# Optimization experiments

Hardware: AMD Instinct MI355X
Metric: run time of the kernel (lower is better)

## Reference

```python
import jax, jax.numpy as jnp
import numpy as np

B, C, N = 4, 256, 2048
H = 8
HD = C // H  # head_dim = 32


def setup_inputs() -> dict:
    key = jax.random.key(0)
    ks = jax.random.split(key, 5)
    s = 1.0 / np.sqrt(C)
    return {
        "x": jax.random.normal(ks[0], (B, C, 3, N), dtype=jnp.float32),
        "Wq": jax.random.normal(ks[1], (C, C), dtype=jnp.float32) * s,
        "Wk": jax.random.normal(ks[2], (C, C), dtype=jnp.float32) * s,
        "Wv": jax.random.normal(ks[3], (C, C), dtype=jnp.float32) * s,
        "Wo": jax.random.normal(ks[4], (C, C), dtype=jnp.float32) * s,
    }


def _vn_linear(W, x):
    # nn.Linear over channel axis: out[b,o,d,n] = sum_c W[o,c] x[b,c,d,n]
    return jnp.einsum('oc,bcdn->bodn', W, x)


def _heads(t):
    # [B,C,3,N] -> [B,H,N,HD,3]
    return t.reshape(B, H, HD, 3, N).transpose(0, 1, 4, 2, 3)


def reference(x, Wq, Wk, Wv, Wo):
    q = _heads(_vn_linear(Wq, x))
    k = _heads(_vn_linear(Wk, x))
    v = _heads(_vn_linear(Wv, x))
    # energy contracts over (head_dim, 3)
    energy = jnp.einsum('bhnci,bhmci->bhnm', q, k)
    attn = jax.nn.softmax(energy / np.sqrt(HD), axis=-1)
    out = jnp.einsum('bhnm,bhmci->bhnci', attn, v)
    # [B,H,N,HD,3] -> [B,C,3,N]
    out = out.transpose(0, 1, 3, 4, 2).reshape(B, C, 3, N)
    out = _vn_linear(Wo, out)
    return out + x
```

## Files before the change

kernel.cpp:

```cpp
#include <hip/hip_runtime.h>
#include <hip/hip_bf16.h>
#include <cmath>


typedef unsigned short u16;
typedef unsigned int   u32;
typedef u16   u16x8  __attribute__((ext_vector_type(8)));
typedef short s16x8  __attribute__((ext_vector_type(8)));
typedef float f32x4  __attribute__((ext_vector_type(4)));
typedef float f32x16 __attribute__((ext_vector_type(16)));

namespace {
constexpr int Nc = 2048, Fc = 96;
constexpr float SCALE_LOG2 = 0.17677669529663687f * 1.4426950408889634f;
constexpr int KP = 104;
constexpr int VP = 40;
constexpr int VOFF = 32 * KP;
constexpr int SBUF = VOFF + 96 * VP;
}

__device__ inline float fast_exp2(float x) {
#if __has_builtin(__builtin_amdgcn_exp2f)
    return __builtin_amdgcn_exp2f(x);
#else
    return exp2f(x);
#endif
}

__device__ inline u16 f2bf(float x) {
    union { float f; unsigned u; } v; v.f = x;
    unsigned r = v.u + 0x7FFFu + ((v.u >> 16) & 1u);
    return (u16)(r >> 16);
}

__global__ __launch_bounds__(256) void wconv_kernel(
    const float* __restrict__ Wq, const float* __restrict__ Wk,
    const float* __restrict__ Wv, const float* __restrict__ Wo,
    u16* __restrict__ Wb)
{
    const int id = blockIdx.x * 256 + threadIdx.x;
    const int base = id * 8;
    const int o = base >> 8, c = base & 255;
    const int sel = o >> 8, ol = o & 255;
    const float* src = (sel == 0) ? Wq : (sel == 1) ? Wk : (sel == 2) ? Wv : Wo;
    const float sc = (sel == 0) ? SCALE_LOG2 : 1.0f;
    const float4 a = *(const float4*)&src[(size_t)ol * 256 + c];
    const float4 b = *(const float4*)&src[(size_t)ol * 256 + c + 4];
    u16x8 r;
    r[0]=f2bf(a.x*sc); r[1]=f2bf(a.y*sc); r[2]=f2bf(a.z*sc); r[3]=f2bf(a.w*sc);
    r[4]=f2bf(b.x*sc); r[5]=f2bf(b.y*sc); r[6]=f2bf(b.z*sc); r[7]=f2bf(b.w*sc);
    *(u16x8*)&Wb[(size_t)o * 256 + c] = r;
}

__global__ __launch_bounds__(256) void xt_kernel(
    const float* __restrict__ x, u16* __restrict__ xt)
{
    const int nt = blockIdx.x, ct = blockIdx.y, bi = blockIdx.z;
    const int b = bi / 3, i = bi % 3;
    const int t = (int)threadIdx.x;
    const int n0 = nt * 64, c0 = ct * 64;

    __shared__ u16 tile[64][72];

    const int n_l = t & 63;
#pragma unroll
    for (int it = 0; it < 16; ++it) {
        const int c_l = (t >> 6) + it * 4;
        tile[n_l][c_l] =
            f2bf(x[(((size_t)(b * 256 + c0 + c_l)) * 3 + i) * Nc + n0 + n_l]);
    }
    __syncthreads();
#pragma unroll
    for (int it = 0; it < 2; ++it) {
        const int idx = t + it * 256;
        const int nn = idx >> 3, part = idx & 7;
        *(u16x8*)&xt[((size_t)bi * Nc + n0 + nn) * 256 + c0 + part * 8] =
            *(const u16x8*)&tile[nn][part * 8];
    }
}

__global__ __launch_bounds__(256) void qkv_gemm_kernel(
    const u16* __restrict__ xt, const u16* __restrict__ wb,
    u16* __restrict__ Qt, u16* __restrict__ Kt, u16* __restrict__ Vf)
{
    const int nt = blockIdx.x;
    const int wy = blockIdx.y;
    const int bi = blockIdx.z;
    const int b = bi / 3, i = bi % 3;
    const int wsel = wy >> 1, ot = wy & 1;

    const u16* xs = xt + ((size_t)bi * Nc + nt * 128) * 256;
    const u16* ws = wb + (size_t)(wsel * 256 + ot * 128) * 256;

    __shared__ u16 xl[128][40];
    __shared__ u16 wl[128][40];

    const int t = (int)threadIdx.x;
    const int wv = t >> 6, lane = t & 63;
    const int g = lane >> 4, c16 = lane & 15;
    const int wr = wv >> 1, wc = wv & 1;

    f32x4 acc[4][4];
#pragma unroll
    for (int mi = 0; mi < 4; ++mi)
#pragma unroll
        for (int ni = 0; ni < 4; ++ni)
#pragma unroll
            for (int r = 0; r < 4; ++r) acc[mi][ni][r] = 0.f;

    for (int ks = 0; ks < 8; ++ks) {
        __syncthreads();
#pragma unroll
        for (int it = 0; it < 2; ++it) {
            const int idx = t + it * 256;
            const int row = idx >> 2, part = idx & 3;
            *(u16x8*)&xl[row][part * 8] =
                *(const u16x8*)&xs[(size_t)row * 256 + ks * 32 + part * 8];
            *(u16x8*)&wl[row][part * 8] =
                *(const u16x8*)&ws[(size_t)row * 256 + ks * 32 + part * 8];
        }
        __syncthreads();

        s16x8 af[4], bf[4];
        if (wsel < 2) {
#pragma unroll
            for (int mi = 0; mi < 4; ++mi) af[mi] = *(const s16x8*)&xl[wr*64 + mi*16 + c16][g*8];
#pragma unroll
            for (int ni = 0; ni < 4; ++ni) bf[ni] = *(const s16x8*)&wl[wc*64 + ni*16 + c16][g*8];
        } else {
#pragma unroll
            for (int mi = 0; mi < 4; ++mi) af[mi] = *(const s16x8*)&wl[wr*64 + mi*16 + c16][g*8];
#pragma unroll
            for (int ni = 0; ni < 4; ++ni) bf[ni] = *(const s16x8*)&xl[wc*64 + ni*16 + c16][g*8];
        }
#pragma unroll
        for (int mi = 0; mi < 4; ++mi)
#pragma unroll
            for (int ni = 0; ni < 4; ++ni)
                acc[mi][ni] = __builtin_amdgcn_mfma_f32_16x16x32_bf16(
                    af[mi], bf[ni], acc[mi][ni], 0, 0, 0);
    }

    if (wsel < 2) {
        u16* dst = wsel ? Kt : Qt;
#pragma unroll
        for (int mi = 0; mi < 4; ++mi)
#pragma unroll
            for (int ni = 0; ni < 4; ++ni) {
                const int o = ot * 128 + wc * 64 + ni * 16 + c16;
                const int h = o >> 5, cw = o & 31;
#pragma unroll
                for (int r = 0; r < 4; ++r) {
                    const int n = nt * 128 + wr * 64 + mi * 16 + g * 4 + r;
                    dst[((size_t)(b * 8 + h) * Nc + n) * Fc + i * 32 + cw] =
                        f2bf(acc[mi][ni][r]);
                }
            }
    } else {
#pragma unroll
        for (int mi = 0; mi < 4; ++mi)
#pragma unroll
            for (int ni = 0; ni < 4; ++ni) {
                const int n = nt * 128 + wc * 64 + ni * 16 + c16;
#pragma unroll
                for (int r = 0; r < 4; ++r) {
                    const int o = ot * 128 + wr * 64 + mi * 16 + g * 4 + r;
                    const int h = o >> 5, cw = o & 31;
                    Vf[((size_t)(b * 8 + h) * Fc + i * 32 + cw) * Nc + n] =
                        f2bf(acc[mi][ni][r]);
                }
            }
    }
}

__global__ __launch_bounds__(256) void attn_mfma_kernel(
    const u16* __restrict__ Qt, const u16* __restrict__ Kt,
    const u16* __restrict__ Vf, u16* __restrict__ aot)
{
    const int bid = (int)blockIdx.x;
    const int lid = (bid & 7) * 64 + (bid >> 3);
    const int bh = lid >> 4;
    const int qt = lid & 15;

    const int t_   = (int)threadIdx.x;
    const int wq   = t_ >> 6;
    const int lane = t_ & 63;
    const int ql   = lane & 31;
    const int hi   = lane >> 5;

    __shared__ u16 sbuf[3 * SBUF];

    const int qb = qt * 128 + wq * 32;

    s16x8 bq[6];
#pragma unroll
    for (int s6 = 0; s6 < 6; ++s6)
        bq[s6] = *(const s16x8*)&Qt[((size_t)bh * Nc + qb + ql) * Fc + s6 * 16 + hi * 8];

    const u16* g_cur[3]; int g_str[3], g_dst[3];
#pragma unroll
    for (int it = 0; it < 3; ++it) {
        const int c = t_ + it * 256;
        if (c < 384) {
            const int row = c / 12, part = c - row * 12;
            g_cur[it] = Kt + ((size_t)bh * Nc + row) * Fc + part * 8;
            g_str[it] = 32 * Fc;
            g_dst[it] = row * KP + part * 8;
        } else {
            const int c2 = c - 384, f = c2 >> 2, part = c2 & 3;
            g_cur[it] = Vf + ((size_t)bh * Fc + f) * Nc + part * 8;
            g_str[it] = 32;
            g_dst[it] = VOFF + f * VP + part * 8;
        }
    }

    f32x16 acc[3];
#pragma unroll
    for (int ft = 0; ft < 3; ++ft)
#pragma unroll
        for (int r = 0; r < 16; ++r) acc[ft][r] = 0.f;
    float lacc[8];
#pragma unroll
    for (int r = 0; r < 8; ++r) lacc[r] = 0.f;

    u16* b0 = sbuf;
    u16* b1 = sbuf + SBUF;
    u16* b2 = sbuf + 2 * SBUF;

    u16x8 sreg[3];
#pragma unroll
    for (int it = 0; it < 3; ++it) { sreg[it] = *(const u16x8*)g_cur[it]; g_cur[it] += g_str[it]; }
#pragma unroll
    for (int it = 0; it < 3; ++it) *(u16x8*)&b0[g_dst[it]] = sreg[it];
#pragma unroll
    for (int it = 0; it < 3; ++it) { sreg[it] = *(const u16x8*)g_cur[it]; g_cur[it] += g_str[it]; }
    __syncthreads();

    f32x16 svE, svO;
#pragma unroll
    for (int r = 0; r < 16; ++r) svE[r] = 0.f;
#pragma unroll
    for (int s6 = 0; s6 < 6; ++s6) {
        const s16x8 ka = *(const s16x8*)&b0[ql * KP + s6 * 16 + hi * 8];
        svE = __builtin_amdgcn_mfma_f32_32x32x16_bf16(ka, bq[s6], svE, 0, 0, 0);
    }
#pragma unroll
    for (int it = 0; it < 3; ++it) *(u16x8*)&b1[g_dst[it]] = sreg[it];
#pragma unroll
    for (int it = 0; it < 3; ++it) { sreg[it] = *(const u16x8*)g_cur[it]; g_cur[it] += g_str[it]; }
    __syncthreads();

    u16 *bA = b0, *bB = b1, *bC = b2;

    auto body = [&](int t, f32x16& SC, f32x16& SN) {
        if (t < 63) {
#pragma unroll
            for (int r = 0; r < 16; ++r) SN[r] = 0.f;
#pragma unroll
            for (int s6 = 0; s6 < 6; ++s6) {
                const s16x8 ka = *(const s16x8*)&bB[ql * KP + s6 * 16 + hi * 8];
                SN = __builtin_amdgcn_mfma_f32_32x32x16_bf16(ka, bq[s6], SN, 0, 0, 0);
            }
        }
        if (t < 62) {
#pragma unroll
            for (int it = 0; it < 3; ++it) *(u16x8*)&bC[g_dst[it]] = sreg[it];
        }
        if (t < 61) {
#pragma unroll
            for (int it = 0; it < 3; ++it) { sreg[it] = *(const u16x8*)g_cur[it]; g_cur[it] += g_str[it]; }
        }

#pragma unroll
        for (int r = 0; r < 16; ++r) SC[r] = fast_exp2(SC[r]);
#pragma unroll
        for (int r = 0; r < 8; ++r) lacc[r] += SC[r] + SC[r + 8];

        u32 pk8[8];
#pragma unroll
        for (int j = 0; j < 8; ++j)
            asm("v_cvt_pk_bf16_f32 %0, %1, %2" : "=v"(pk8[j]) : "v"(SC[2*j]), "v"(SC[2*j+1]));
        asm volatile("v_permlane32_swap_b32 %0, %1" : "+v"(pk8[0]), "+v"(pk8[2]));
        asm volatile("v_permlane32_swap_b32 %0, %1" : "+v"(pk8[1]), "+v"(pk8[3]));
        asm volatile("v_permlane32_swap_b32 %0, %1" : "+v"(pk8[4]), "+v"(pk8[6]));
        asm volatile("v_permlane32_swap_b32 %0, %1" : "+v"(pk8[5]), "+v"(pk8[7]));
        union U { u32 w[4]; s16x8 v; } pb0, pb1;
        pb0.w[0]=pk8[0]; pb0.w[1]=pk8[1]; pb0.w[2]=pk8[2]; pb0.w[3]=pk8[3];
        pb1.w[0]=pk8[4]; pb1.w[1]=pk8[5]; pb1.w[2]=pk8[6]; pb1.w[3]=pk8[7];

#pragma unroll
        for (int ft = 0; ft < 3; ++ft) {
            const s16x8 va0 = *(const s16x8*)&bA[VOFF + (ft * 32 + ql) * VP + hi * 8];
            acc[ft] = __builtin_amdgcn_mfma_f32_32x32x16_bf16(va0, pb0.v, acc[ft], 0, 0, 0);
            const s16x8 va1 = *(const s16x8*)&bA[VOFF + (ft * 32 + ql) * VP + 16 + hi * 8];
            acc[ft] = __builtin_amdgcn_mfma_f32_32x32x16_bf16(va1, pb1.v, acc[ft], 0, 0, 0);
        }

        if (t < 63) __syncthreads();
    };

    for (int tb = 0; tb < 32; ++tb) {
        body(2 * tb, svE, svO);
        { u16* tmp = bA; bA = bB; bB = bC; bC = tmp; }
        body(2 * tb + 1, svO, svE);
        { u16* tmp = bA; bA = bB; bB = bC; bC = tmp; }
    }

    float l4[4];
#pragma unroll
    for (int r = 0; r < 4; ++r) l4[r] = lacc[r] + lacc[r + 4];
    const float l2a = l4[0] + l4[2], l2b = l4[1] + l4[3];
    float l_s = l2a + l2b;
    l_s += __shfl_xor(l_s, 32);
    const float inv = 1.f / l_s;

    __syncthreads();
    u16* ot = sbuf + wq * 3328;
#pragma unroll
    for (int ft = 0; ft < 3; ++ft)
#pragma unroll
        for (int r = 0; r < 16; ++r) {
            const int frow = (r & 3) + 8 * (r >> 2) + 4 * hi;
            ot[ql * 104 + ft * 32 + frow] = f2bf(acc[ft][r] * inv);
        }
    __syncthreads();

    u16x8 v6[6];
#pragma unroll
    for (int j = 0; j < 6; ++j)
        v6[j] = *(const u16x8*)&ot[ql * 104 + hi * 48 + j * 8];

    const int n = qb + ql;
    const int b_ = bh >> 3, h_ = bh & 7;
    const size_t base0 = ((size_t)(b_ * 3 + 0) * Nc + n) * 256 + h_ * 32;
    const size_t base1 = ((size_t)(b_ * 3 + 1) * Nc + n) * 256 + h_ * 32;
    const size_t base2 = ((size_t)(b_ * 3 + 2) * Nc + n) * 256 + h_ * 32;
    if (hi == 0) {
        *(u16x8*)&aot[base0 +  0] = v6[0];
        *(u16x8*)&aot[base0 +  8] = v6[1];
        *(u16x8*)&aot[base0 + 16] = v6[2];
        *(u16x8*)&aot[base0 + 24] = v6[3];
        *(u16x8*)&aot[base1 +  0] = v6[4];
        *(u16x8*)&aot[base1 +  8] = v6[5];
    } else {
        *(u16x8*)&aot[base1 + 16] = v6[0];
        *(u16x8*)&aot[base1 + 24] = v6[1];
        *(u16x8*)&aot[base2 +  0] = v6[2];
        *(u16x8*)&aot[base2 +  8] = v6[3];
        *(u16x8*)&aot[base2 + 16] = v6[4];
        *(u16x8*)&aot[base2 + 24] = v6[5];
    }
}

__global__ __launch_bounds__(256) void out_gemm_kernel(
    const u16* __restrict__ aot, const u16* __restrict__ wb,
    const float* __restrict__ x, float* __restrict__ out)
{
    const int nt = blockIdx.x, ot = blockIdx.y, bi = blockIdx.z;
    const int b = bi / 3, i = bi % 3;

    const u16* bs = aot + ((size_t)bi * Nc + nt * 128) * 256;
    const u16* ws = wb + (size_t)(768 + ot * 128) * 256;

    __shared__ u16 al[128][40];
    __shared__ u16 wl[128][40];

    const int t = (int)threadIdx.x;
    const int wv = t >> 6, lane = t & 63;
    const int g = lane >> 4, c16 = lane & 15;
    const int wr = wv >> 1, wc = wv & 1;

    f32x4 acc[4][4];
#pragma unroll
    for (int mi = 0; mi < 4; ++mi)
#pragma unroll
        for (int ni = 0; ni < 4; ++ni)
#pragma unroll
            for (int r = 0; r < 4; ++r) acc[mi][ni][r] = 0.f;

    for (int ks = 0; ks < 8; ++ks) {
        __syncthreads();
#pragma unroll
        for (int it = 0; it < 2; ++it) {
            const int idx = t + it * 256;
            const int row = idx >> 2, part = idx & 3;
            *(u16x8*)&al[row][part * 8] =
                *(const u16x8*)&bs[(size_t)row * 256 + ks * 32 + part * 8];
            *(u16x8*)&wl[row][part * 8] =
                *(const u16x8*)&ws[(size_t)row * 256 + ks * 32 + part * 8];
        }
        __syncthreads();

        s16x8 af[4], bf[4];
#pragma unroll
        for (int mi = 0; mi < 4; ++mi) af[mi] = *(const s16x8*)&wl[wr*64 + mi*16 + c16][g*8];
#pragma unroll
        for (int ni = 0; ni < 4; ++ni) bf[ni] = *(const s16x8*)&al[wc*64 + ni*16 + c16][g*8];
#pragma unroll
        for (int mi = 0; mi < 4; ++mi)
#pragma unroll
            for (int ni = 0; ni < 4; ++ni)
                acc[mi][ni] = __builtin_amdgcn_mfma_f32_16x16x32_bf16(
                    af[mi], bf[ni], acc[mi][ni], 0, 0, 0);
    }

#pragma unroll
    for (int mi = 0; mi < 4; ++mi)
#pragma unroll
        for (int ni = 0; ni < 4; ++ni) {
            const int n = nt * 128 + wc * 64 + ni * 16 + c16;
#pragma unroll
            for (int r = 0; r < 4; ++r) {
                const int o = ot * 128 + wr * 64 + mi * 16 + g * 4 + r;
                const size_t idx = ((size_t)(b * 256 + o) * 3 + i) * Nc + n;
                out[idx] = x[idx] + acc[mi][ni][r];
            }
        }
}

extern "C" void kernel_launch(void* const* d_in, const int* in_sizes, int n_in,
                              void* d_out, int out_size, void* d_ws, size_t ws_size,
                              hipStream_t stream) {
    const float* x  = (const float*)d_in[0];
    const float* Wq = (const float*)d_in[1];
    const float* Wk = (const float*)d_in[2];
    const float* Wv = (const float*)d_in[3];
    const float* Wo = (const float*)d_in[4];
    float* out = (float*)d_out;

    const size_t E = (size_t)32 * Fc * Nc;
    u16* xt  = (u16*)d_ws;
    u16* wbw = xt + E;
    u16* qt  = wbw + 262144;
    u16* kt  = qt + E;
    u16* vf  = kt + E;
    u16* aot = vf + E;

    dim3 blk(256);
    wconv_kernel    <<<dim3(128),        blk, 0, stream>>>(Wq, Wk, Wv, Wo, wbw);
    xt_kernel       <<<dim3(32, 4, 12),  blk, 0, stream>>>(x, xt);
    qkv_gemm_kernel <<<dim3(16, 6, 12),  blk, 0, stream>>>(xt, wbw, qt, kt, vf);
    attn_mfma_kernel<<<dim3(512),        blk, 0, stream>>>(qt, kt, vf, aot);
    out_gemm_kernel <<<dim3(16, 2, 12),  blk, 0, stream>>>(aot, wbw, x, out);
}
```

Before: 124.9 us.

## Split attention over two key halves and merge partials in a combine kernel

The attention kernel now splits the key range into two halves, launching twice as many blocks that each process 1024 keys, and writes unnormalized-then-normalized partial outputs plus row sums to workspace. A new combine kernel weights the two partials by their softmax sums and writes the head-interleaved layout consumed by the output GEMM. The K/V pipeline is simplified from triple to double buffering with a launch bound hint for higher occupancy. This raises parallelism on 256 CUs but adds an extra kernel launch, extra global traffic for partials, and bf16 rounding of partials.

```diff
diff --git a/kernel.cpp b/kernel.cpp
--- a/kernel.cpp
+++ b/kernel.cpp
@@ -31,6 +31,10 @@
     union { float f; unsigned u; } v; v.f = x;
     unsigned r = v.u + 0x7FFFu + ((v.u >> 16) & 1u);
     return (u16)(r >> 16);
+}
+
+__device__ inline float bf2f(u16 x) {
+    union { unsigned u; float f; } v; v.u = ((unsigned)x) << 16; return v.f;
 }
 
 __global__ __launch_bounds__(256) void wconv_kernel(
@@ -173,14 +177,16 @@
     }
 }
 
-__global__ __launch_bounds__(256) void attn_mfma_kernel(
+__global__ __launch_bounds__(256, 4) void attn_mfma_kernel(
     const u16* __restrict__ Qt, const u16* __restrict__ Kt,
-    const u16* __restrict__ Vf, u16* __restrict__ aot)
+    const u16* __restrict__ Vf, u16* __restrict__ Ob, float* __restrict__ lP)
 {
     const int bid = (int)blockIdx.x;
-    const int lid = (bid & 7) * 64 + (bid >> 3);
-    const int bh = lid >> 4;
-    const int qt = lid & 15;
+    const int lid = (bid & 7) * 128 + (bid >> 3);
+    const int bh   = lid >> 5;
+    const int r5   = lid & 31;
+    const int qt   = r5 >> 1;
+    const int half = r5 & 1;
 
     const int t_   = (int)threadIdx.x;
     const int wq   = t_ >> 6;
@@ -188,9 +194,10 @@
     const int ql   = lane & 31;
     const int hi   = lane >> 5;
 
-    __shared__ u16 sbuf[3 * SBUF];
+    __shared__ u16 sbuf[2 * SBUF];
 
     const int qb = qt * 128 + wq * 32;
+    const int k0 = half * 1024;
 
     s16x8 bq[6];
 #pragma unroll
@@ -203,12 +210,12 @@
         const int c = t_ + it * 256;
         if (c < 384) {
             const int row = c / 12, part = c - row * 12;
-            g_cur[it] = Kt + ((size_t)bh * Nc + row) * Fc + part * 8;
+            g_cur[it] = Kt + ((size_t)bh * Nc + k0 + row) * Fc + part * 8;
             g_str[it] = 32 * Fc;
             g_dst[it] = row * KP + part * 8;
         } else {
             const int c2 = c - 384, f = c2 >> 2, part = c2 & 3;
-            g_cur[it] = Vf + ((size_t)bh * Fc + f) * Nc + part * 8;
+            g_cur[it] = Vf + ((size_t)bh * Fc + f) * Nc + k0 + part * 8;
             g_str[it] = 32;
             g_dst[it] = VOFF + f * VP + part * 8;
         }
@@ -223,63 +230,46 @@
 #pragma unroll
     for (int r = 0; r < 8; ++r) lacc[r] = 0.f;
 
-    u16* b0 = sbuf;
-    u16* b1 = sbuf + SBUF;
-    u16* b2 = sbuf + 2 * SBUF;
+    u16* bA = sbuf;
+    u16* bB = sbuf + SBUF;
 
     u16x8 sreg[3];
 #pragma unroll
     for (int it = 0; it < 3; ++it) { sreg[it] = *(const u16x8*)g_cur[it]; g_cur[it] += g_str[it]; }
 #pragma unroll
-    for (int it = 0; it < 3; ++it) *(u16x8*)&b0[g_dst[it]] = sreg[it];
+    for (int it = 0; it < 3; ++it) *(u16x8*)&bA[g_dst[it]] = sreg[it];
 #pragma unroll
     for (int it = 0; it < 3; ++it) { sreg[it] = *(const u16x8*)g_cur[it]; g_cur[it] += g_str[it]; }
     __syncthreads();
 
-    f32x16 svE, svO;
-#pragma unroll
-    for (int r = 0; r < 16; ++r) svE[r] = 0.f;
-#pragma unroll
-    for (int s6 = 0; s6 < 6; ++s6) {
-        const s16x8 ka = *(const s16x8*)&b0[ql * KP + s6 * 16 + hi * 8];
-        svE = __builtin_amdgcn_mfma_f32_32x32x16_bf16(ka, bq[s6], svE, 0, 0, 0);
-    }
-#pragma unroll
-    for (int it = 0; it < 3; ++it) *(u16x8*)&b1[g_dst[it]] = sreg[it];
-#pragma unroll
-    for (int it = 0; it < 3; ++it) { sreg[it] = *(const u16x8*)g_cur[it]; g_cur[it] += g_str[it]; }
-    __syncthreads();
-
-    u16 *bA = b0, *bB = b1, *bC = b2;
-
-    auto body = [&](int t, f32x16& SC, f32x16& SN) {
-        if (t < 63) {
-#pragma unroll
-            for (int r = 0; r < 16; ++r) SN[r] = 0.f;
-#pragma unroll
-            for (int s6 = 0; s6 < 6; ++s6) {
-                const s16x8 ka = *(const s16x8*)&bB[ql * KP + s6 * 16 + hi * 8];
-                SN = __builtin_amdgcn_mfma_f32_32x32x16_bf16(ka, bq[s6], SN, 0, 0, 0);
-            }
-        }
-        if (t < 62) {
-#pragma unroll
-            for (int it = 0; it < 3; ++it) *(u16x8*)&bC[g_dst[it]] = sreg[it];
-        }
-        if (t < 61) {
+    for (int kt = 0; kt < 32; ++kt) {
+        if (kt < 31) {
+#pragma unroll
+            for (int it = 0; it < 3; ++it) *(u16x8*)&bB[g_dst[it]] = sreg[it];
+        }
+        if (kt < 30) {
 #pragma unroll
             for (int it = 0; it < 3; ++it) { sreg[it] = *(const u16x8*)g_cur[it]; g_cur[it] += g_str[it]; }
         }
 
-#pragma unroll
-        for (int r = 0; r < 16; ++r) SC[r] = fast_exp2(SC[r]);
-#pragma unroll
-        for (int r = 0; r < 8; ++r) lacc[r] += SC[r] + SC[r + 8];
+        f32x16 sv;
+#pragma unroll
+        for (int r = 0; r < 16; ++r) sv[r] = 0.f;
+#pragma unroll
+        for (int s6 = 0; s6 < 6; ++s6) {
+            const s16x8 ka = *(const s16x8*)&bA[ql * KP + s6 * 16 + hi * 8];
+            sv = __builtin_amdgcn_mfma_f32_32x32x16_bf16(ka, bq[s6], sv, 0, 0, 0);
+        }
+
+#pragma unroll
+        for (int r = 0; r < 16; ++r) sv[r] = fast_exp2(sv[r]);
+#pragma unroll
+        for (int r = 0; r < 8; ++r) lacc[r] += sv[r] + sv[r + 8];
 
         u32 pk8[8];
 #pragma unroll
         for (int j = 0; j < 8; ++j)
-            asm("v_cvt_pk_bf16_f32 %0, %1, %2" : "=v"(pk8[j]) : "v"(SC[2*j]), "v"(SC[2*j+1]));
+            asm("v_cvt_pk_bf16_f32 %0, %1, %2" : "=v"(pk8[j]) : "v"(sv[2*j]), "v"(sv[2*j+1]));
         asm volatile("v_permlane32_swap_b32 %0, %1" : "+v"(pk8[0]), "+v"(pk8[2]));
         asm volatile("v_permlane32_swap_b32 %0, %1" : "+v"(pk8[1]), "+v"(pk8[3]));
         asm volatile("v_permlane32_swap_b32 %0, %1" : "+v"(pk8[4]), "+v"(pk8[6]));
@@ -296,59 +286,68 @@
             acc[ft] = __builtin_amdgcn_mfma_f32_32x32x16_bf16(va1, pb1.v, acc[ft], 0, 0, 0);
         }
 
-        if (t < 63) __syncthreads();
-    };
-
-    for (int tb = 0; tb < 32; ++tb) {
-        body(2 * tb, svE, svO);
-        { u16* tmp = bA; bA = bB; bB = bC; bC = tmp; }
-        body(2 * tb + 1, svO, svE);
-        { u16* tmp = bA; bA = bB; bB = bC; bC = tmp; }
+        if (kt < 31) __syncthreads();
+        { u16* tmp = bA; bA = bB; bB = tmp; }
     }
 
     float l4[4];
 #pragma unroll
     for (int r = 0; r < 4; ++r) l4[r] = lacc[r] + lacc[r + 4];
-    const float l2a = l4[0] + l4[2], l2b = l4[1] + l4[3];
-    float l_s = l2a + l2b;
+    float l_s = (l4[0] + l4[2]) + (l4[1] + l4[3]);
     l_s += __shfl_xor(l_s, 32);
     const float inv = 1.f / l_s;
 
-    __syncthreads();
-    u16* ot = sbuf + wq * 3328;
+    u16* dst = Ob + (((size_t)half * 32 + bh) * Fc) * Nc;
 #pragma unroll
     for (int ft = 0; ft < 3; ++ft)
 #pragma unroll
         for (int r = 0; r < 16; ++r) {
             const int frow = (r & 3) + 8 * (r >> 2) + 4 * hi;
-            ot[ql * 104 + ft * 32 + frow] = f2bf(acc[ft][r] * inv);
-        }
+            dst[(size_t)(ft * 32 + frow) * Nc + qb + ql] = f2bf(acc[ft][r] * inv);
+        }
+    if (hi == 0)
+        lP[((size_t)half * 32 + bh) * Nc + qb + ql] = l_s;
+}
+
+__global__ __launch_bounds__(256) void combine_kernel(
+    const u16* __restrict__ Ob, const float* __restrict__ lP,
+    u16* __restrict__ aot)
+{
+    const int nt = blockIdx.x;
+    const int bh = blockIdx.y;
+    const int t = (int)threadIdx.x;
+    const int n0 = nt * 64;
+    const int b = bh >> 3, h = bh & 7;
+
+    __shared__ float wgt[64];
+    __shared__ u16 tile[64][104];
+
+    if (t < 64) {
+        const float l0 = lP[(size_t)bh * Nc + n0 + t];
+        const float l1 = lP[((size_t)32 + bh) * Nc + n0 + t];
+        wgt[t] = l0 / (l0 + l1);
+    }
     __syncthreads();
 
-    u16x8 v6[6];
-#pragma unroll
-    for (int j = 0; j < 6; ++j)
-        v6[j] = *(const u16x8*)&ot[ql * 104 + hi * 48 + j * 8];
-
-    const int n = qb + ql;
-    const int b_ = bh >> 3, h_ = bh & 7;
-    const size_t base0 = ((size_t)(b_ * 3 + 0) * Nc + n) * 256 + h_ * 32;
-    const size_t base1 = ((size_t)(b_ * 3 + 1) * Nc + n) * 256 + h_ * 32;
-    const size_t base2 = ((size_t)(b_ * 3 + 2) * Nc + n) * 256 + h_ * 32;
-    if (hi == 0) {
-        *(u16x8*)&aot[base0 +  0] = v6[0];
-        *(u16x8*)&aot[base0 +  8] = v6[1];
-        *(u16x8*)&aot[base0 + 16] = v6[2];
-        *(u16x8*)&aot[base0 + 24] = v6[3];
-        *(u16x8*)&aot[base1 +  0] = v6[4];
-        *(u16x8*)&aot[base1 +  8] = v6[5];
-    } else {
-        *(u16x8*)&aot[base1 + 16] = v6[0];
-        *(u16x8*)&aot[base1 + 24] = v6[1];
-        *(u16x8*)&aot[base2 +  0] = v6[2];
-        *(u16x8*)&aot[base2 +  8] = v6[3];
-        *(u16x8*)&aot[base2 + 16] = v6[4];
-        *(u16x8*)&aot[base2 + 24] = v6[5];
+    const int q = t & 63;
+    const int fw = t >> 6;
+    const u16* p0 = Ob + ((size_t)bh * Fc) * Nc;
+    const u16* p1 = Ob + (((size_t)32 + bh) * Fc) * Nc;
+    const float w0 = wgt[q];
+#pragma unroll
+    for (int it = 0; it < 24; ++it) {
+        const int f = it * 4 + fw;
+        const float a0 = bf2f(p0[(size_t)f * Nc + n0 + q]);
+        const float a1 = bf2f(p1[(size_t)f * Nc + n0 + q]);
+        tile[q][f] = f2bf(a0 * w0 + a1 * (1.f - w0));
+    }
+    __syncthreads();
+
+    const int nn = t >> 2, part = t & 3;
+#pragma unroll
+    for (int i = 0; i < 3; ++i) {
+        *(u16x8*)&aot[((size_t)(b * 3 + i) * Nc + n0 + nn) * 256 + h * 32 + part * 8] =
+            *(const u16x8*)&tile[nn][i * 32 + part * 8];
     }
 }
 
@@ -434,12 +433,15 @@
     u16* qt  = wbw + 262144;
     u16* kt  = qt + E;
     u16* vf  = kt + E;
-    u16* aot = vf + E;
+    u16* obp = vf + E;
+    float* lP = (float*)(obp + 2 * E);
+    u16* aot = xt;
 
     dim3 blk(256);
     wconv_kernel    <<<dim3(128),        blk, 0, stream>>>(Wq, Wk, Wv, Wo, wbw);
     xt_kernel       <<<dim3(32, 4, 12),  blk, 0, stream>>>(x, xt);
     qkv_gemm_kernel <<<dim3(16, 6, 12),  blk, 0, stream>>>(xt, wbw, qt, kt, vf);
-    attn_mfma_kernel<<<dim3(512),        blk, 0, stream>>>(qt, kt, vf, aot);
+    attn_mfma_kernel<<<dim3(1024),       blk, 0, stream>>>(qt, kt, vf, obp, lP);
+    combine_kernel  <<<dim3(32, 32),     blk, 0, stream>>>(obp, lP, aot);
     out_gemm_kernel <<<dim3(16, 2, 12),  blk, 0, stream>>>(aot, wbw, x, out);
 }
```

Result: slower. 138.8 us (+11.1%).

## Split attention over key halves and merge partial outputs in output GEMM

Applied to the files above, without the earlier changes.

Splits each attention block's key range into two halves, doubling the grid from 512 to 1024 blocks. Each half writes a separately normalized partial output and its softmax row sum. The output GEMM loader then combines the two partials, weighted by their row sums, before the Wo projection. The aim is better occupancy across the CUs. The cost is twice the partial-output memory traffic, plus extra conversion work and lP loads in the GEMM loader. The merge is valid because softmax uses no running-max subtraction, so both halves share the same scale.

```diff
diff --git a/kernel.cpp b/kernel.cpp
--- a/kernel.cpp
+++ b/kernel.cpp
@@ -31,6 +31,10 @@
     union { float f; unsigned u; } v; v.f = x;
     unsigned r = v.u + 0x7FFFu + ((v.u >> 16) & 1u);
     return (u16)(r >> 16);
+}
+
+__device__ inline float bf2f(u16 x) {
+    union { unsigned u; float f; } v; v.u = ((unsigned)x) << 16; return v.f;
 }
 
 __global__ __launch_bounds__(256) void wconv_kernel(
@@ -175,12 +179,14 @@
 
 __global__ __launch_bounds__(256) void attn_mfma_kernel(
     const u16* __restrict__ Qt, const u16* __restrict__ Kt,
-    const u16* __restrict__ Vf, u16* __restrict__ aot)
+    const u16* __restrict__ Vf, u16* __restrict__ obt, float* __restrict__ lP)
 {
     const int bid = (int)blockIdx.x;
-    const int lid = (bid & 7) * 64 + (bid >> 3);
-    const int bh = lid >> 4;
-    const int qt = lid & 15;
+    const int lid = (bid & 7) * 128 + (bid >> 3);
+    const int bh   = lid >> 5;
+    const int r5   = lid & 31;
+    const int qt   = r5 >> 1;
+    const int half = r5 & 1;
 
     const int t_   = (int)threadIdx.x;
     const int wq   = t_ >> 6;
@@ -191,6 +197,7 @@
     __shared__ u16 sbuf[3 * SBUF];
 
     const int qb = qt * 128 + wq * 32;
+    const int k0 = half * 1024;
 
     s16x8 bq[6];
 #pragma unroll
@@ -203,12 +210,12 @@
         const int c = t_ + it * 256;
         if (c < 384) {
             const int row = c / 12, part = c - row * 12;
-            g_cur[it] = Kt + ((size_t)bh * Nc + row) * Fc + part * 8;
+            g_cur[it] = Kt + ((size_t)bh * Nc + k0 + row) * Fc + part * 8;
             g_str[it] = 32 * Fc;
             g_dst[it] = row * KP + part * 8;
         } else {
             const int c2 = c - 384, f = c2 >> 2, part = c2 & 3;
-            g_cur[it] = Vf + ((size_t)bh * Fc + f) * Nc + part * 8;
+            g_cur[it] = Vf + ((size_t)bh * Fc + f) * Nc + k0 + part * 8;
             g_str[it] = 32;
             g_dst[it] = VOFF + f * VP + part * 8;
         }
@@ -253,7 +260,7 @@
     u16 *bA = b0, *bB = b1, *bC = b2;
 
     auto body = [&](int t, f32x16& SC, f32x16& SN) {
-        if (t < 63) {
+        if (t < 31) {
 #pragma unroll
             for (int r = 0; r < 16; ++r) SN[r] = 0.f;
 #pragma unroll
@@ -262,11 +269,11 @@
                 SN = __builtin_amdgcn_mfma_f32_32x32x16_bf16(ka, bq[s6], SN, 0, 0, 0);
             }
         }
-        if (t < 62) {
+        if (t < 30) {
 #pragma unroll
             for (int it = 0; it < 3; ++it) *(u16x8*)&bC[g_dst[it]] = sreg[it];
         }
-        if (t < 61) {
+        if (t < 29) {
 #pragma unroll
             for (int it = 0; it < 3; ++it) { sreg[it] = *(const u16x8*)g_cur[it]; g_cur[it] += g_str[it]; }
         }
@@ -296,10 +303,10 @@
             acc[ft] = __builtin_amdgcn_mfma_f32_32x32x16_bf16(va1, pb1.v, acc[ft], 0, 0, 0);
         }
 
-        if (t < 63) __syncthreads();
+        if (t < 31) __syncthreads();
     };
 
-    for (int tb = 0; tb < 32; ++tb) {
+    for (int tb = 0; tb < 16; ++tb) {
         body(2 * tb, svE, svO);
         { u16* tmp = bA; bA = bB; bB = bC; bC = tmp; }
         body(2 * tb + 1, svO, svE);
@@ -309,10 +316,11 @@
     float l4[4];
 #pragma unroll
     for (int r = 0; r < 4; ++r) l4[r] = lacc[r] + lacc[r + 4];
-    const float l2a = l4[0] + l4[2], l2b = l4[1] + l4[3];
-    float l_s = l2a + l2b;
+    float l_s = (l4[0] + l4[2]) + (l4[1] + l4[3]);
     l_s += __shfl_xor(l_s, 32);
     const float inv = 1.f / l_s;
+    if (hi == 0)
+        lP[((size_t)half * 32 + bh) * Nc + qb + ql] = l_s;
 
     __syncthreads();
     u16* ot = sbuf + wq * 3328;
@@ -332,34 +340,36 @@
 
     const int n = qb + ql;
     const int b_ = bh >> 3, h_ = bh & 7;
-    const size_t base0 = ((size_t)(b_ * 3 + 0) * Nc + n) * 256 + h_ * 32;
-    const size_t base1 = ((size_t)(b_ * 3 + 1) * Nc + n) * 256 + h_ * 32;
-    const size_t base2 = ((size_t)(b_ * 3 + 2) * Nc + n) * 256 + h_ * 32;
+    const size_t base0 = (((size_t)half * 12 + b_ * 3 + 0) * Nc + n) * 256 + h_ * 32;
+    const size_t base1 = (((size_t)half * 12 + b_ * 3 + 1) * Nc + n) * 256 + h_ * 32;
+    const size_t base2 = (((size_t)half * 12 + b_ * 3 + 2) * Nc + n) * 256 + h_ * 32;
     if (hi == 0) {
-        *(u16x8*)&aot[base0 +  0] = v6[0];
-        *(u16x8*)&aot[base0 +  8] = v6[1];
-        *(u16x8*)&aot[base0 + 16] = v6[2];
-        *(u16x8*)&aot[base0 + 24] = v6[3];
-        *(u16x8*)&aot[base1 +  0] = v6[4];
-        *(u16x8*)&aot[base1 +  8] = v6[5];
+        *(u16x8*)&obt[base0 +  0] = v6[0];
+        *(u16x8*)&obt[base0 +  8] = v6[1];
+        *(u16x8*)&obt[base0 + 16] = v6[2];
+        *(u16x8*)&obt[base0 + 24] = v6[3];
+        *(u16x8*)&obt[base1 +  0] = v6[4];
+        *(u16x8*)&obt[base1 +  8] = v6[5];
     } else {
-        *(u16x8*)&aot[base1 + 16] = v6[0];
-        *(u16x8*)&aot[base1 + 24] = v6[1];
-        *(u16x8*)&aot[base2 +  0] = v6[2];
-        *(u16x8*)&aot[base2 +  8] = v6[3];
-        *(u16x8*)&aot[base2 + 16] = v6[4];
-        *(u16x8*)&aot[base2 + 24] = v6[5];
+        *(u16x8*)&obt[base1 + 16] = v6[0];
+        *(u16x8*)&obt[base1 + 24] = v6[1];
+        *(u16x8*)&obt[base2 +  0] = v6[2];
+        *(u16x8*)&obt[base2 +  8] = v6[3];
+        *(u16x8*)&obt[base2 + 16] = v6[4];
+        *(u16x8*)&obt[base2 + 24] = v6[5];
     }
 }
 
 __global__ __launch_bounds__(256) void out_gemm_kernel(
-    const u16* __restrict__ aot, const u16* __restrict__ wb,
-    const float* __restrict__ x, float* __restrict__ out)
+    const u16* __restrict__ obt, const float* __restrict__ lP,
+    const u16* __restrict__ wb, const float* __restrict__ x,
+    float* __restrict__ out)
 {
     const int nt = blockIdx.x, ot = blockIdx.y, bi = blockIdx.z;
     const int b = bi / 3, i = bi % 3;
 
-    const u16* bs = aot + ((size_t)bi * Nc + nt * 128) * 256;
+    const u16* p0 = obt + ((size_t)bi * Nc) * 256;
+    const u16* p1 = obt + (((size_t)12 + bi) * Nc) * 256;
     const u16* ws = wb + (size_t)(768 + ot * 128) * 256;
 
     __shared__ u16 al[128][40];
@@ -384,8 +394,18 @@
         for (int it = 0; it < 2; ++it) {
             const int idx = t + it * 256;
             const int row = idx >> 2, part = idx & 3;
-            *(u16x8*)&al[row][part * 8] =
-                *(const u16x8*)&bs[(size_t)row * 256 + ks * 32 + part * 8];
+            const int n = nt * 128 + row;
+            const float l0 = lP[((size_t)(b * 8 + ks)) * Nc + n];
+            const float l1 = lP[((size_t)(32 + b * 8 + ks)) * Nc + n];
+            const float w0 = l0 / (l0 + l1);
+            const float w1 = 1.f - w0;
+            const u16x8 a0 = *(const u16x8*)&p0[(size_t)n * 256 + ks * 32 + part * 8];
+            const u16x8 a1 = *(const u16x8*)&p1[(size_t)n * 256 + ks * 32 + part * 8];
+            u16x8 rr;
+#pragma unroll
+            for (int j = 0; j < 8; ++j)
+                rr[j] = f2bf(bf2f(a0[j]) * w0 + bf2f(a1[j]) * w1);
+            *(u16x8*)&al[row][part * 8] = rr;
             *(u16x8*)&wl[row][part * 8] =
                 *(const u16x8*)&ws[(size_t)row * 256 + ks * 32 + part * 8];
         }
@@ -434,12 +454,13 @@
     u16* qt  = wbw + 262144;
     u16* kt  = qt + E;
     u16* vf  = kt + E;
-    u16* aot = vf + E;
+    u16* obt = vf + E;
+    float* lP = (float*)(obt + 2 * E);
 
     dim3 blk(256);
     wconv_kernel    <<<dim3(128),        blk, 0, stream>>>(Wq, Wk, Wv, Wo, wbw);
     xt_kernel       <<<dim3(32, 4, 12),  blk, 0, stream>>>(x, xt);
     qkv_gemm_kernel <<<dim3(16, 6, 12),  blk, 0, stream>>>(xt, wbw, qt, kt, vf);
-    attn_mfma_kernel<<<dim3(512),        blk, 0, stream>>>(qt, kt, vf, aot);
-    out_gemm_kernel <<<dim3(16, 2, 12),  blk, 0, stream>>>(aot, wbw, x, out);
-}
+    attn_mfma_kernel<<<dim3(1024),       blk, 0, stream>>>(qt, kt, vf, obt, lP);
+    out_gemm_kernel <<<dim3(16, 2, 12),  blk, 0, stream>>>(obt, lP, wbw, x, out);
+}
```

Result: faster. 120.6 us (-3.5%).
